# Performance work log

Measured on AMD Instinct MI355X. Metric: run time of the kernel, lower is better.

Reference implementation:

```python
import jax, jax.numpy as jnp
import numpy as np
from jax import lax

STRIDE, PAD, DIL = 1, 1, 1  # main deform-conv hyperparams


def setup_inputs() -> dict:
    key = jax.random.key(0)
    k1, k2, k3, k4, k5 = jax.random.split(key, 5)
    B, C_in, C_out, L, K = 8, 256, 256, 4096, 3
    x = jax.random.normal(k1, (B, C_in, L), dtype=jnp.float32)
    # offset-field conv1d params (kernel 3, pad 1, produces C_in offset channels)
    offset_w = jax.random.normal(k2, (C_in, C_in, 3), dtype=jnp.float32) * 0.02
    offset_b = jax.random.normal(k3, (C_in,), dtype=jnp.float32) * 0.02
    # main deform conv params
    weight = jax.random.normal(k4, (C_out, C_in, K), dtype=jnp.float32) * 0.02
    bias = jax.random.normal(k5, (C_out,), dtype=jnp.float32) * 0.02
    return {"x": x, "offset_w": offset_w, "offset_b": offset_b, "weight": weight, "bias": bias}


def _deform_conv1d(x, offset_w, offset_b, weight, bias):
    B, C, L = x.shape
    K = weight.shape[-1]
    # offset field: Conv1d(C -> C, k=3, pad=1), one offset per channel per position
    off = lax.conv_general_dilated(
        x, offset_w, window_strides=(1,), padding=[(1, 1)],
        dimension_numbers=("NCH", "OIH", "NCH")) + offset_b[None, :, None]
    L_out = off.shape[-1]
    # base sampling grid: pos(k, p) = p*stride - pad + k*dil  -> [K, L_out]
    base = (jnp.arange(L_out, dtype=x.dtype) * STRIDE - PAD)[None, :] \
         + (jnp.arange(K, dtype=x.dtype) * DIL)[:, None]
    pos = base[None, None] + off[:, :, None, :]          # [B, C, K, L_out]
    p0 = jnp.floor(pos)
    w1 = pos - p0                                         # linear-interp weight
    i0 = p0.astype(jnp.int32)
    i1 = i0 + 1
    xb = jnp.broadcast_to(x[:, :, None, :], pos.shape)    # [B, C, K, L]
    g0 = jnp.take_along_axis(xb, jnp.clip(i0, 0, L - 1), axis=-1)
    g1 = jnp.take_along_axis(xb, jnp.clip(i1, 0, L - 1), axis=-1)
    zero = jnp.zeros((), x.dtype)
    v0 = jnp.where((i0 >= 0) & (i0 < L), g0, zero)
    v1 = jnp.where((i1 >= 0) & (i1 < L), g1, zero)
    sampled = v0 * (1 - w1) + v1 * w1                     # [B, C, K, L_out]
    out = jnp.einsum("ock,bckl->bol", weight, sampled) + bias[None, :, None]
    return out


def reference(x, offset_w, offset_b, weight, bias):
    return _deform_conv1d(x, offset_w, offset_b, weight, bias)
```

## Files before the change

kernel.cpp:

```cpp
#include <hip/hip_runtime.h>
#include <hip/hip_bf16.h>

#define B_  8
#define C_  256
#define L_  4096
#define KD_ 768
#define XPW 4112
#define TW  104
#define TSZ (128 * TW)

typedef __attribute__((ext_vector_type(8))) __bf16 bf16x8;
typedef __attribute__((ext_vector_type(4))) float f32x4;
typedef __attribute__((ext_vector_type(8))) unsigned short u16x8;
typedef __attribute__((ext_vector_type(2))) unsigned int u32x2;

__device__ __forceinline__ unsigned short f2bf(float f){
  union { float f; unsigned u; } v; v.f = f;
  unsigned r = v.u + 0x7fffu + ((v.u >> 16) & 1u);
  return (unsigned short)(r >> 16);
}
__device__ __forceinline__ float bf2f(unsigned short h){
  union { unsigned u; float f; } v; v.u = ((unsigned)h) << 16;
  return v.f;
}
__device__ __forceinline__ unsigned pk2bf(float lo, float hi){
  __hip_bfloat162 h2 = __float22bfloat162_rn(make_float2(lo, hi));
  unsigned u;
  __builtin_memcpy(&u, &h2, 4);
  return u;
}

__device__ __forceinline__ void stage_tile26k(const unsigned short* __restrict__ g,
                                              unsigned short* l, int t){
  int wid = t >> 6, lane = t & 63;
  #pragma unroll
  for (int s = 0; s < 3; ++s){
    int seg = wid + s * 8;
    const char* src = (const char*)g + seg * 1024 + lane * 16;
    char* dst = (char*)l + seg * 1024;
    __builtin_amdgcn_global_load_lds(
        (const __attribute__((address_space(1))) unsigned int*)src,
        (__attribute__((address_space(3))) unsigned int*)dst, 16, 0, 0);
  }
  if (wid < 2){
    int seg = 24 + wid;
    const char* src = (const char*)g + seg * 1024 + lane * 16;
    char* dst = (char*)l + seg * 1024;
    __builtin_amdgcn_global_load_lds(
        (const __attribute__((address_space(1))) unsigned int*)src,
        (__attribute__((address_space(3))) unsigned int*)dst, 16, 0, 0);
  }
}

__global__ __launch_bounds__(256) void prep(const float* __restrict__ offw,
                                            const float* __restrict__ w,
                                            const float* __restrict__ x,
                                            unsigned short* __restrict__ wO,
                                            unsigned short* __restrict__ wM,
                                            unsigned short* __restrict__ xpad){
  int blk = blockIdx.x;
  if (blk < 768){
    int idx = blk * 256 + threadIdx.x;
    int r = idx / KD_, rem = idx % KD_;
    int rt = r >> 7, row = r & 127;
    int ch = rem / 96, col = rem % 96;
    int pos = (rt * 8 + ch) * TSZ + row * TW + col;
    wO[pos] = f2bf(offw[idx]);
    wM[pos] = f2bf(w[idx]);
  } else {
    int row = blk - 768;
    const float4* src = reinterpret_cast<const float4*>(x + (size_t)row * L_);
    unsigned short* dr = xpad + (size_t)row * XPW;
    int tid = threadIdx.x;
    #pragma unroll
    for (int q = 0; q < 2; ++q){
      float4 f0 = src[tid * 4 + q * 2];
      float4 f1 = src[tid * 4 + q * 2 + 1];
      u16x8 h;
      h[0]=f2bf(f0.x); h[1]=f2bf(f0.y); h[2]=f2bf(f0.z); h[3]=f2bf(f0.w);
      h[4]=f2bf(f1.x); h[5]=f2bf(f1.y); h[6]=f2bf(f1.z); h[7]=f2bf(f1.w);
      *reinterpret_cast<u16x8*>(dr + 8 + tid * 16 + q * 8) = h;
    }
    if (tid < 2){
      u16x8 z = {};
      *reinterpret_cast<u16x8*>(dr + (tid == 0 ? 0 : 8 + L_)) = z;
    }
  }
}

template <int MODE, int PADDED>
__global__ __launch_bounds__(512, 6) void dconv_gemm(
    const void* __restrict__ xsrc,
    const unsigned short* __restrict__ wT,
    const float* __restrict__ bvec,
    const unsigned short* __restrict__ off_in,
    void* __restrict__ outp){
  __shared__ __align__(16) unsigned short As[TSZ];
  __shared__ __align__(16) unsigned short Bs[TSZ];

  int bid = blockIdx.x;
  int wk = (bid & 7) * 64 + (bid >> 3);
  int b  = wk >> 6;
  int yt = (wk >> 5) & 1;
  int lt = wk & 31;
  int l0 = lt * 128, m0 = yt * 128;

  int t = threadIdx.x, lane = t & 63, wid = t >> 6;
  int wm = wid >> 1, wn = wid & 1;
  const unsigned short* xbh = PADDED
      ? (const unsigned short*)xsrc + (size_t)b * C_ * XPW + 8
      : nullptr;
  const float* xbf = PADDED ? nullptr
      : (const float*)xsrc + (size_t)b * C_ * L_;
  const unsigned short* offp = off_in + (size_t)b * C_ * L_;
  const unsigned short* wBase = wT + (size_t)yt * 8 * TSZ;
  f32x4 acc[2][4] = {};

  int lrow = t & 127;
  int l = l0 + lrow;
  int cphase = t >> 7;

  for (int ch = 0; ch < 8; ++ch){
    stage_tile26k(wBase + (size_t)ch * TSZ, As, t);
    int cin = ch * 32;
    #pragma unroll
    for (int it = 0; it < 2; ++it){
      int q = it * 4 + cphase;
      int colb = q * 12;
      if (PADDED && !MODE){
        unsigned hv[12];
        #pragma unroll
        for (int u = 0; u < 4; ++u){
          const unsigned short* xr = xbh + (size_t)(cin + q * 4 + u) * XPW + (l - 1);
          hv[u*3+0] = xr[0]; hv[u*3+1] = xr[1]; hv[u*3+2] = xr[2];
        }
        #pragma unroll
        for (int p = 0; p < 3; ++p){
          u32x2 dw;
          dw.x = hv[4*p+0] | (hv[4*p+1] << 16);
          dw.y = hv[4*p+2] | (hv[4*p+3] << 16);
          *reinterpret_cast<u32x2*>(&Bs[lrow * TW + colb + p * 4]) = dw;
        }
      } else {
        float s[12];
        #pragma unroll
        for (int u = 0; u < 4; ++u){
          int c = cin + q * 4 + u;
          int i0; float w1;
          if (MODE){
            float off = bf2f(offp[(size_t)c * L_ + l]);
            float pos = (float)(l - 1) + off;
            if (PADDED) pos = fminf(fmaxf(pos, -6.f), (float)(L_ + 4));
            float p0 = floorf(pos);
            w1 = pos - p0; i0 = (int)p0;
          } else { i0 = l - 1; w1 = 0.f; }
          float w0 = 1.f - w1;
          if (PADDED){
            const unsigned short* xr = xbh + (size_t)c * XPW + i0;
            float v0 = bf2f(xr[0]), v1 = bf2f(xr[1]), v2 = bf2f(xr[2]), v3 = bf2f(xr[3]);
            s[u*3+0] = v0 * w0 + v1 * w1;
            s[u*3+1] = v1 * w0 + v2 * w1;
            s[u*3+2] = v2 * w0 + v3 * w1;
          } else {
            const float* xr = xbf + (size_t)c * L_;
            float v[4];
            #pragma unroll
            for (int j = 0; j < 4; ++j){
              int ix = i0 + j;
              v[j] = (MODE || j < 3) && ((unsigned)ix < (unsigned)L_) ? xr[ix] : 0.f;
            }
            #pragma unroll
            for (int k = 0; k < 3; ++k)
              s[u*3+k] = MODE ? (v[k] * w0 + v[k+1] * w1) : v[k];
          }
        }
        #pragma unroll
        for (int p = 0; p < 3; ++p){
          u32x2 dw;
          dw.x = pk2bf(s[4*p+0], s[4*p+1]);
          dw.y = pk2bf(s[4*p+2], s[4*p+3]);
          *reinterpret_cast<u32x2*>(&Bs[lrow * TW + colb + p * 4]) = dw;
        }
      }
    }
    __syncthreads();
    #pragma unroll
    for (int kf = 0; kf < 3; ++kf){
      int col = kf * 32 + (lane >> 4) * 8;
      bf16x8 af[2], bfv[4];
      #pragma unroll
      for (int mi = 0; mi < 2; ++mi)
        af[mi] = __builtin_bit_cast(bf16x8,
          *reinterpret_cast<const u16x8*>(&As[(wm * 32 + mi * 16 + (lane & 15)) * TW + col]));
      #pragma unroll
      for (int ni = 0; ni < 4; ++ni)
        bfv[ni] = __builtin_bit_cast(bf16x8,
          *reinterpret_cast<const u16x8*>(&Bs[(wn * 64 + ni * 16 + (lane & 15)) * TW + col]));
      #pragma unroll
      for (int mi = 0; mi < 2; ++mi)
        #pragma unroll
        for (int ni = 0; ni < 4; ++ni)
          acc[mi][ni] = __builtin_amdgcn_mfma_f32_16x16x32_bf16(af[mi], bfv[ni], acc[mi][ni], 0, 0, 0);
    }
    __syncthreads();
  }

  int rg = lane >> 4, cx = lane & 15;
  if (MODE == 0){
    unsigned short* ob = (unsigned short*)outp + (size_t)b * C_ * L_;
    #pragma unroll
    for (int mi = 0; mi < 2; ++mi)
      #pragma unroll
      for (int r = 0; r < 4; ++r){
        int c = m0 + wm * 32 + mi * 16 + rg * 4 + r;
        float bv = bvec[c];
        #pragma unroll
        for (int ni = 0; ni < 4; ++ni){
          int ll = l0 + wn * 64 + ni * 16 + cx;
          ob[(size_t)c * L_ + ll] = f2bf(acc[mi][ni][r] + bv);
        }
      }
  } else {
    float* ob = (float*)outp + (size_t)b * C_ * L_;
    #pragma unroll
    for (int mi = 0; mi < 2; ++mi)
      #pragma unroll
      for (int r = 0; r < 4; ++r){
        int o = m0 + wm * 32 + mi * 16 + rg * 4 + r;
        float bv = bvec[o];
        #pragma unroll
        for (int ni = 0; ni < 4; ++ni){
          int ll = l0 + wn * 64 + ni * 16 + cx;
          ob[(size_t)o * L_ + ll] = acc[mi][ni][r] + bv;
        }
      }
  }
}

extern "C" void kernel_launch(void* const* d_in, const int* in_sizes, int n_in,
                              void* d_out, int out_size, void* d_ws, size_t ws_size,
                              hipStream_t stream){
  (void)in_sizes; (void)n_in; (void)out_size;
  const float* x   = (const float*)d_in[0];
  const float* ow  = (const float*)d_in[1];
  const float* obv = (const float*)d_in[2];
  const float* w   = (const float*)d_in[3];
  const float* bv  = (const float*)d_in[4];
  float* out = (float*)d_out;

  unsigned short* wO     = (unsigned short*)d_ws;
  unsigned short* wM     = wO + 2 * 8 * TSZ;
  unsigned short* off_ws = wM + 2 * 8 * TSZ;
  unsigned short* xpad   = off_ws + (size_t)B_ * C_ * L_;
  size_t need = (char*)(xpad + (size_t)B_ * C_ * XPW) - (char*)d_ws;
  bool pad_ok = ws_size >= need;

  prep<<<dim3(pad_ok ? 768 + 2048 : 768), dim3(256), 0, stream>>>(
      ow, w, x, wO, wM, xpad);
  dim3 blk(512), grd(512);
  if (pad_ok){
    dconv_gemm<0,1><<<grd, blk, 0, stream>>>(xpad, wO, obv, off_ws, off_ws);
    dconv_gemm<1,1><<<grd, blk, 0, stream>>>(xpad, wM, bv, off_ws, out);
  } else {
    dconv_gemm<0,0><<<grd, blk, 0, stream>>>(x, wO, obv, off_ws, off_ws);
    dconv_gemm<1,0><<<grd, blk, 0, stream>>>(x, wM, bv, off_ws, out);
  }
}
```

Baseline: 73.06 us.

## Replace padded LDS tiles with XOR-swizzled 128-wide layout

Switches the A and B shared-memory tiles from a padded row stride of 104 elements to a 128-element row with an XOR swizzle on the column, applied consistently in weight prep, staging, B-tile writes and MFMA fragment reads. B-tile writes rotate the channel-group order per row to spread LDS bank accesses. The goal is to remove bank conflicts on LDS reads and writes. The cost is larger tiles (64KB per block), so occupancy hints drop from 6 to 4 blocks and more global bytes are staged, about a quarter of which are padding.

```diff
diff --git a/kernel.cpp b/kernel.cpp
--- a/kernel.cpp
+++ b/kernel.cpp
@@ -6,8 +6,6 @@
 #define L_  4096
 #define KD_ 768
 #define XPW 4112
-#define TW  104
-#define TSZ (128 * TW)
 
 typedef __attribute__((ext_vector_type(8))) __bf16 bf16x8;
 typedef __attribute__((ext_vector_type(4))) float f32x4;
@@ -30,20 +28,16 @@
   return u;
 }
 
-__device__ __forceinline__ void stage_tile26k(const unsigned short* __restrict__ g,
+__device__ __forceinline__ int swz(int row, int col){
+  return (row << 7) + (col ^ ((row & 15) << 3));
+}
+
+__device__ __forceinline__ void stage_tile32k(const unsigned short* __restrict__ g,
                                               unsigned short* l, int t){
   int wid = t >> 6, lane = t & 63;
   #pragma unroll
-  for (int s = 0; s < 3; ++s){
-    int seg = wid + s * 8;
-    const char* src = (const char*)g + seg * 1024 + lane * 16;
-    char* dst = (char*)l + seg * 1024;
-    __builtin_amdgcn_global_load_lds(
-        (const __attribute__((address_space(1))) unsigned int*)src,
-        (__attribute__((address_space(3))) unsigned int*)dst, 16, 0, 0);
-  }
-  if (wid < 2){
-    int seg = 24 + wid;
+  for (int s = 0; s < 4; ++s){
+    int seg = wid * 4 + s;
     const char* src = (const char*)g + seg * 1024 + lane * 16;
     char* dst = (char*)l + seg * 1024;
     __builtin_amdgcn_global_load_lds(
@@ -64,7 +58,7 @@
     int r = idx / KD_, rem = idx % KD_;
     int rt = r >> 7, row = r & 127;
     int ch = rem / 96, col = rem % 96;
-    int pos = (rt * 8 + ch) * TSZ + row * TW + col;
+    int pos = (rt * 8 + ch) * 16384 + swz(row, col);
     wO[pos] = f2bf(offw[idx]);
     wM[pos] = f2bf(w[idx]);
   } else {
@@ -89,14 +83,14 @@
 }
 
 template <int MODE, int PADDED>
-__global__ __launch_bounds__(512, 6) void dconv_gemm(
+__global__ __launch_bounds__(512, 4) void dconv_gemm(
     const void* __restrict__ xsrc,
     const unsigned short* __restrict__ wT,
     const float* __restrict__ bvec,
     const unsigned short* __restrict__ off_in,
     void* __restrict__ outp){
-  __shared__ __align__(16) unsigned short As[TSZ];
-  __shared__ __align__(16) unsigned short Bs[TSZ];
+  __shared__ __align__(16) unsigned short As[16384];
+  __shared__ __align__(16) unsigned short Bs[16384];
 
   int bid = blockIdx.x;
   int wk = (bid & 7) * 64 + (bid >> 3);
@@ -113,19 +107,20 @@
   const float* xbf = PADDED ? nullptr
       : (const float*)xsrc + (size_t)b * C_ * L_;
   const unsigned short* offp = off_in + (size_t)b * C_ * L_;
-  const unsigned short* wBase = wT + (size_t)yt * 8 * TSZ;
+  const unsigned short* wBase = wT + (size_t)yt * 8 * 16384;
   f32x4 acc[2][4] = {};
 
   int lrow = t & 127;
   int l = l0 + lrow;
   int cphase = t >> 7;
+  int rot = (cphase + lrow) & 3;
 
   for (int ch = 0; ch < 8; ++ch){
-    stage_tile26k(wBase + (size_t)ch * TSZ, As, t);
+    stage_tile32k(wBase + (size_t)ch * 16384, As, t);
     int cin = ch * 32;
     #pragma unroll
     for (int it = 0; it < 2; ++it){
-      int q = it * 4 + cphase;
+      int q = it * 4 + rot;
       int colb = q * 12;
       if (PADDED && !MODE){
         unsigned hv[12];
@@ -139,7 +134,7 @@
           u32x2 dw;
           dw.x = hv[4*p+0] | (hv[4*p+1] << 16);
           dw.y = hv[4*p+2] | (hv[4*p+3] << 16);
-          *reinterpret_cast<u32x2*>(&Bs[lrow * TW + colb + p * 4]) = dw;
+          *reinterpret_cast<u32x2*>(&Bs[swz(lrow, colb + p * 4)]) = dw;
         }
       } else {
         float s[12];
@@ -179,7 +174,7 @@
           u32x2 dw;
           dw.x = pk2bf(s[4*p+0], s[4*p+1]);
           dw.y = pk2bf(s[4*p+2], s[4*p+3]);
-          *reinterpret_cast<u32x2*>(&Bs[lrow * TW + colb + p * 4]) = dw;
+          *reinterpret_cast<u32x2*>(&Bs[swz(lrow, colb + p * 4)]) = dw;
         }
       }
     }
@@ -191,11 +186,11 @@
       #pragma unroll
       for (int mi = 0; mi < 2; ++mi)
         af[mi] = __builtin_bit_cast(bf16x8,
-          *reinterpret_cast<const u16x8*>(&As[(wm * 32 + mi * 16 + (lane & 15)) * TW + col]));
+          *reinterpret_cast<const u16x8*>(&As[swz(wm * 32 + mi * 16 + (lane & 15), col)]));
       #pragma unroll
       for (int ni = 0; ni < 4; ++ni)
         bfv[ni] = __builtin_bit_cast(bf16x8,
-          *reinterpret_cast<const u16x8*>(&Bs[(wn * 64 + ni * 16 + (lane & 15)) * TW + col]));
+          *reinterpret_cast<const u16x8*>(&Bs[swz(wn * 64 + ni * 16 + (lane & 15), col)]));
       #pragma unroll
       for (int mi = 0; mi < 2; ++mi)
         #pragma unroll
@@ -249,8 +244,8 @@
   float* out = (float*)d_out;
 
   unsigned short* wO     = (unsigned short*)d_ws;
-  unsigned short* wM     = wO + 2 * 8 * TSZ;
-  unsigned short* off_ws = wM + 2 * 8 * TSZ;
+  unsigned short* wM     = wO + 2 * 8 * 16384;
+  unsigned short* off_ws = wM + 2 * 8 * 16384;
   unsigned short* xpad   = off_ws + (size_t)B_ * C_ * L_;
   size_t need = (char*)(xpad + (size_t)B_ * C_ * XPW) - (char*)d_ws;
   bool pad_ok = ws_size >= need;
```

New measurement: 111.2 us. +52.2%, slower.
